# Performance work log

Hardware: AMD Instinct MI355X
Metric: run time of the kernel (lower is better)

Reference implementation:

```python
import jax, jax.numpy as jnp
import numpy as np

NUM_TOKENS = 200


def setup_inputs() -> dict:
    key = jax.random.key(0)
    ks = jax.random.split(key, 4)
    B, N, D, H, O = 16, 4096, 1024, 512, 4096
    x = jax.random.normal(ks[0], (B, N, D), dtype=jnp.float32)
    W1 = jax.random.normal(ks[1], (H, D), dtype=jnp.float32) * (1.0 / np.sqrt(D))
    b1 = jnp.zeros((H,), dtype=jnp.float32)
    W2 = jax.random.normal(ks[2], (1, H), dtype=jnp.float32) * (1.0 / np.sqrt(H))
    b2 = jnp.zeros((1,), dtype=jnp.float32)
    Wp = jax.random.normal(ks[3], (O, D), dtype=jnp.float32) * (1.0 / np.sqrt(D))
    bp = jnp.zeros((O,), dtype=jnp.float32)
    return {"x": x, "W1": W1, "b1": b1, "W2": W2, "b2": b2, "Wp": Wp, "bp": bp}


def reference(x, W1, b1, W2, b2, Wp, bp):
    # score MLP: Linear(D, D//2) -> GELU(exact) -> Linear(D//2, 1)
    h = jax.nn.gelu(jnp.einsum('bnd,hd->bnh', x, W1) + b1, approximate=False)
    scores = jnp.einsum('bnh,oh->bno', h, W2)[..., 0] + b2[0]  # [B, N]
    # topk (sorted descending, matching torch.topk defaults)
    _, topk_idx = jax.lax.top_k(scores, NUM_TOKENS)  # [B, K]
    # gather selected tokens: [B, K, D]
    select_tokens = jnp.take_along_axis(x, topk_idx[:, :, None], axis=1)
    # final projection
    return jnp.einsum('bkd,od->bko', select_tokens, Wp) + bp
```

## Files before the change

kernel.cpp:

```cpp
#include <hip/hip_runtime.h>
#include <cmath>

#define BB 16
#define NN 4096
#define DD 1024
#define HH 512
#define OO 4096
#define KSEL 200
#define NCAND 256
#define NT (BB * NN)
#define NSLOT (BB * NCAND)

typedef __bf16 bf16x8 __attribute__((ext_vector_type(8)));
typedef float floatx4 __attribute__((ext_vector_type(4)));

__device__ __forceinline__ unsigned short f2b(float f) {
    union { float f; unsigned u; } v; v.f = f;
    unsigned r = v.u + 0x7fffu + ((v.u >> 16) & 1u);
    return (unsigned short)(r >> 16);
}
__device__ __forceinline__ unsigned pk2(float lo, float hi) {
    return (unsigned)f2b(lo) | ((unsigned)f2b(hi) << 16);
}

__device__ __forceinline__ float fast_gelu(float u) {
    float z = u * fmaf(0.0713548162726f, u * u, 1.5957691216f);
    float e = __expf(z);
    float r = __builtin_amdgcn_rcpf(e + 1.0f);
    return u - u * r;
}

__device__ __forceinline__ void gl16(const void* g, void* l) {
    __builtin_amdgcn_global_load_lds(
        (const __attribute__((address_space(1))) unsigned int*)g,
        (__attribute__((address_space(3))) unsigned int*)l, 16, 0, 0);
}

__global__ __launch_bounds__(256) void convert_bf16(
    const float* __restrict__ src, unsigned short* __restrict__ dst, int n8)
{
    int i = blockIdx.x * 256 + threadIdx.x;
    if (i >= n8) return;
    float4 a = ((const float4*)src)[2 * i];
    float4 b = ((const float4*)src)[2 * i + 1];
    uint4 o = make_uint4(pk2(a.x, a.y), pk2(a.z, a.w), pk2(b.x, b.y), pk2(b.z, b.w));
    ((uint4*)dst)[i] = o;
}

#define BK 64
#define NSCORE_BLK ((HH / 128) * (NT / 128))

__global__ __launch_bounds__(256) void score_mfma(
    const unsigned short* __restrict__ xb, const unsigned short* __restrict__ W1b,
    const float* __restrict__ b1, const float* __restrict__ W2,
    float* __restrict__ partials)
{
    __shared__ __align__(16) unsigned short As[128 * BK];
    __shared__ __align__(16) unsigned short Bs[128 * BK];
    __shared__ float red[2][128];

    const int tid = threadIdx.x;
    const int bid = blockIdx.x;
    const int swz = (bid & 7) * (NSCORE_BLK / 8) + (bid >> 3);
    const int ht = swz & 3;
    const int h0 = ht * 128;
    const int t0 = (swz >> 2) * 128;

    const int lane = tid & 63;
    const int w = tid >> 6;
    const int wr = w & 1, wc = w >> 1;
    const int l15 = lane & 15, q = lane >> 4;

    const int srow = tid >> 3;
    const int cb = (tid & 7) ^ (srow & 7);
    const unsigned short* pA[4];
    const unsigned short* pB[4];
#pragma unroll
    for (int i = 0; i < 4; ++i) {
        pA[i] = xb  + (size_t)(t0 + i * 32 + srow) * DD + cb * 8;
        pB[i] = W1b + (size_t)(h0 + i * 32 + srow) * DD + cb * 8;
    }

    floatx4 acc[4][4];
#pragma unroll
    for (int mi = 0; mi < 4; ++mi)
#pragma unroll
        for (int ni = 0; ni < 4; ++ni) acc[mi][ni] = (floatx4){0.f, 0.f, 0.f, 0.f};

    for (int kc = 0; kc < DD; kc += BK) {
        __syncthreads();
#pragma unroll
        for (int i = 0; i < 4; ++i) {
            gl16(pA[i] + kc, &As[(i * 256 + w * 64) * 8]);
            gl16(pB[i] + kc, &Bs[(i * 256 + w * 64) * 8]);
        }
        __syncthreads();
#pragma unroll
        for (int kk = 0; kk < BK; kk += 32) {
            const int kb = kk >> 3;
            bf16x8 af[4], bf[4];
#pragma unroll
            for (int mi = 0; mi < 4; ++mi) {
                const int r = wr * 64 + mi * 16 + l15;
                af[mi] = *(const bf16x8*)&As[r * BK + (((kb + q) ^ (r & 7)) << 3)];
            }
#pragma unroll
            for (int ni = 0; ni < 4; ++ni) {
                const int r = wc * 64 + ni * 16 + l15;
                bf[ni] = *(const bf16x8*)&Bs[r * BK + (((kb + q) ^ (r & 7)) << 3)];
            }
#pragma unroll
            for (int mi = 0; mi < 4; ++mi)
#pragma unroll
                for (int ni = 0; ni < 4; ++ni)
                    acc[mi][ni] = __builtin_amdgcn_mfma_f32_16x16x32_bf16(af[mi], bf[ni], acc[mi][ni], 0, 0, 0);
        }
    }

    float s[4][4];
#pragma unroll
    for (int mi = 0; mi < 4; ++mi)
#pragma unroll
        for (int r = 0; r < 4; ++r) s[mi][r] = 0.f;
#pragma unroll
    for (int ni = 0; ni < 4; ++ni) {
        const int n = h0 + wc * 64 + ni * 16 + l15;
        const float bias = b1[n];
        const float w2v = W2[n];
#pragma unroll
        for (int mi = 0; mi < 4; ++mi)
#pragma unroll
            for (int r = 0; r < 4; ++r) {
                float u = acc[mi][ni][r] + bias;
                s[mi][r] = fmaf(fast_gelu(u), w2v, s[mi][r]);
            }
    }
#pragma unroll
    for (int mi = 0; mi < 4; ++mi)
#pragma unroll
        for (int r = 0; r < 4; ++r) {
#pragma unroll
            for (int off = 1; off < 16; off <<= 1)
                s[mi][r] += __shfl_xor(s[mi][r], off, 64);
        }
    __syncthreads();
    if (l15 == 0) {
#pragma unroll
        for (int mi = 0; mi < 4; ++mi)
#pragma unroll
            for (int r = 0; r < 4; ++r)
                red[wc][wr * 64 + mi * 16 + q * 4 + r] = s[mi][r];
    }
    __syncthreads();
    if (tid < 128)
        partials[(size_t)ht * NT + t0 + tid] = red[0][tid] + red[1][tid];
}

__global__ __launch_bounds__(256) void cand_select(
    const float* __restrict__ partials, int* __restrict__ cand)
{
    __shared__ unsigned uk[NN];
    __shared__ int hist[256];
    __shared__ int eq[64];
    __shared__ int sh_pref, sh_rk, sh_cntgt, sh_eqcnt;
    const int b = blockIdx.x, tid = threadIdx.x;

    for (int i = tid; i < NN; i += 256) {
        const int t = b * NN + i;
        float v = partials[t] + partials[NT + t] + partials[2 * NT + t] + partials[3 * NT + t];
        union { float f; unsigned u; } c; c.f = v;
        uk[i] = (c.u & 0x80000000u) ? ~c.u : (c.u | 0x80000000u);
    }
    if (tid == 0) { sh_pref = 0; sh_rk = NCAND; }
    __syncthreads();

    for (int sh = 24; sh >= 0; sh -= 8) {
        hist[tid] = 0;
        __syncthreads();
        const unsigned pref = (unsigned)sh_pref;
        for (int i = tid; i < NN; i += 256) {
            unsigned k = uk[i];
            bool match = (sh == 24) || (((k ^ pref) >> (sh + 8)) == 0);
            if (match) atomicAdd(&hist[(k >> sh) & 255], 1);
        }
        __syncthreads();
        if (tid == 0) {
            int rk = sh_rk, cum = 0;
            for (int bin = 255; bin >= 0; --bin) {
                int c = hist[bin];
                if (cum + c >= rk) { sh_pref = (int)(pref | ((unsigned)bin << sh)); sh_rk = rk - cum; break; }
                cum += c;
            }
        }
        __syncthreads();
    }
    const unsigned T = (unsigned)sh_pref;
    if (tid == 0) { sh_cntgt = 0; sh_eqcnt = 0; }
    cand[b * NCAND + tid] = 0;
    __syncthreads();
    for (int i = tid; i < NN; i += 256) {
        unsigned k = uk[i];
        if (k > T) {
            int p = atomicAdd(&sh_cntgt, 1);
            if (p < NCAND) cand[b * NCAND + p] = i;
        } else if (k == T) {
            int p = atomicAdd(&sh_eqcnt, 1);
            if (p < 64) eq[p] = i;
        }
    }
    __syncthreads();
    if (tid == 0) {
        int cg = sh_cntgt; if (cg > NCAND) cg = NCAND;
        int ec = sh_eqcnt; if (ec > 64) ec = 64;
        int need = NCAND - cg; if (need > ec) need = ec; if (need < 0) need = 0;
        for (int a = 1; a < ec; ++a) {
            int v = eq[a]; int j = a - 1;
            while (j >= 0 && eq[j] > v) { eq[j + 1] = eq[j]; --j; }
            eq[j + 1] = v;
        }
        for (int j = 0; j < need; ++j) cand[b * NCAND + cg + j] = eq[j];
    }
}

#define RT 64
#define RLDP 68

__global__ __launch_bounds__(256) void rescore_kernel(
    const float* __restrict__ x, const int* __restrict__ cand,
    const float* __restrict__ W1, const float* __restrict__ b1,
    const float* __restrict__ W2, float* __restrict__ pc)
{
    __shared__ float As[16][RLDP];
    __shared__ float Bs[16][RLDP];
    __shared__ int rowbase[RT];

    const int tid = threadIdx.x;
    const int s0 = blockIdx.x * RT;
    const int h0 = blockIdx.y * RT;
    const int tx = tid & 15;
    const int ty = tid >> 4;
    const int lr = tid >> 2;
    const int lq = tid & 3;

    if (tid < RT) {
        const int slot = s0 + tid;
        rowbase[tid] = (slot >> 8) * NN + (cand[slot] & (NN - 1));
    }
    __syncthreads();

    const float* Arow = x + (size_t)rowbase[lr] * DD;
    const float* Brow = W1 + (size_t)(h0 + lr) * DD;

    float acc[4][4];
#pragma unroll
    for (int i = 0; i < 4; ++i)
#pragma unroll
        for (int j = 0; j < 4; ++j) acc[i][j] = 0.0f;

    for (int kc = 0; kc < DD; kc += 16) {
        float4 a = *(const float4*)(Arow + kc + lq * 4);
        float4 wv = *(const float4*)(Brow + kc + lq * 4);
        __syncthreads();
        As[lq * 4 + 0][lr] = a.x; As[lq * 4 + 1][lr] = a.y;
        As[lq * 4 + 2][lr] = a.z; As[lq * 4 + 3][lr] = a.w;
        Bs[lq * 4 + 0][lr] = wv.x; Bs[lq * 4 + 1][lr] = wv.y;
        Bs[lq * 4 + 2][lr] = wv.z; Bs[lq * 4 + 3][lr] = wv.w;
        __syncthreads();
#pragma unroll
        for (int kk = 0; kk < 16; ++kk) {
            float ra[4], rb[4];
            *(float4*)&ra[0] = *(const float4*)&As[kk][ty * 4];
            *(float4*)&rb[0] = *(const float4*)&Bs[kk][tx * 4];
#pragma unroll
            for (int i = 0; i < 4; ++i)
#pragma unroll
                for (int j = 0; j < 4; ++j)
                    acc[i][j] = fmaf(ra[i], rb[j], acc[i][j]);
        }
    }

    float s[4];
#pragma unroll
    for (int i = 0; i < 4; ++i) s[i] = 0.0f;
#pragma unroll
    for (int j = 0; j < 4; ++j) {
        const int h = h0 + tx * 4 + j;
        const float bias = b1[h];
        const float w2v = W2[h];
#pragma unroll
        for (int i = 0; i < 4; ++i) {
            float u = acc[i][j] + bias;
            float g = 0.5f * u * (1.0f + erff(u * 0.70710678118654752440f));
            s[i] = fmaf(g, w2v, s[i]);
        }
    }
#pragma unroll
    for (int i = 0; i < 4; ++i) {
#pragma unroll
        for (int off = 8; off > 0; off >>= 1)
            s[i] += __shfl_down(s[i], off, 16);
    }
    if (tx == 0) {
#pragma unroll
        for (int i = 0; i < 4; ++i)
            pc[(size_t)blockIdx.y * NSLOT + s0 + ty * 4 + i] = s[i];
    }
}

__global__ __launch_bounds__(256) void final_topk(
    const float* __restrict__ pc, const int* __restrict__ cand,
    int* __restrict__ topk)
{
    __shared__ unsigned long long keys[NCAND];
    const int b = blockIdx.x, tid = threadIdx.x;
    const int slot = b * NCAND + tid;
    float es = 0.f;
#pragma unroll
    for (int g = 0; g < 8; ++g) es += pc[(size_t)g * NSLOT + slot];
    const int tok = cand[slot];
    union { float f; unsigned u; } c; c.f = es;
    unsigned mono = (c.u & 0x80000000u) ? ~c.u : (c.u | 0x80000000u);
    keys[tid] = ((unsigned long long)mono << 12) | (unsigned)(4095 - tok);
    __syncthreads();

    for (int k = 2; k <= NCAND; k <<= 1) {
        for (int j = k >> 1; j > 0; j >>= 1) {
            const int p = tid ^ j;
            const unsigned long long a = keys[tid];
            const unsigned long long o = keys[p];
            const unsigned long long hi = a > o ? a : o;
            const unsigned long long lo = a > o ? o : a;
            const unsigned long long nv = ((tid < p) == ((tid & k) == 0)) ? hi : lo;
            __syncthreads();
            keys[tid] = nv;
            __syncthreads();
        }
    }
    if (tid < KSEL) topk[b * KSEL + tid] = 4095 - (int)(keys[tid] & 4095u);
}

#define NPROJ_BLK (((BB * KSEL) / 128) * (OO / 128))

__global__ __launch_bounds__(256) void proj_mfma(
    const unsigned short* __restrict__ xb, const int* __restrict__ topk,
    const unsigned short* __restrict__ Wpb, const float* __restrict__ bp,
    float* __restrict__ out)
{
    __shared__ __align__(16) unsigned short As[128 * BK];
    __shared__ __align__(16) unsigned short Bs[128 * BK];
    __shared__ int rowbase[128];

    const int tid = threadIdx.x;
    const int bid = blockIdx.x;
    const int swz = (bid & 7) * (NPROJ_BLK / 8) + (bid >> 3);
    const int r0 = (swz >> 5) * 128;
    const int o0 = (swz & 31) * 128;
    const int lane = tid & 63;
    const int w = tid >> 6;
    const int wr = w & 1, wc = w >> 1;
    const int l15 = lane & 15, q = lane >> 4;

    if (tid < 128) {
        const int r = r0 + tid;
        rowbase[tid] = (r / KSEL) * NN + (topk[r] & (NN - 1));
    }
    __syncthreads();

    const int srow = tid >> 3;
    const int cb = (tid & 7) ^ (srow & 7);
    const unsigned short* pA[4];
    const unsigned short* pB[4];
#pragma unroll
    for (int i = 0; i < 4; ++i) {
        pA[i] = xb  + (size_t)rowbase[i * 32 + srow] * DD + cb * 8;
        pB[i] = Wpb + (size_t)(o0 + i * 32 + srow) * DD + cb * 8;
    }

    floatx4 acc[4][4];
#pragma unroll
    for (int mi = 0; mi < 4; ++mi)
#pragma unroll
        for (int ni = 0; ni < 4; ++ni) acc[mi][ni] = (floatx4){0.f, 0.f, 0.f, 0.f};

    for (int kc = 0; kc < DD; kc += BK) {
        __syncthreads();
#pragma unroll
        for (int i = 0; i < 4; ++i) {
            gl16(pA[i] + kc, &As[(i * 256 + w * 64) * 8]);
            gl16(pB[i] + kc, &Bs[(i * 256 + w * 64) * 8]);
        }
        __syncthreads();
#pragma unroll
        for (int kk = 0; kk < BK; kk += 32) {
            const int kb = kk >> 3;
            bf16x8 af[4], bf[4];
#pragma unroll
            for (int mi = 0; mi < 4; ++mi) {
                const int r = wr * 64 + mi * 16 + l15;
                af[mi] = *(const bf16x8*)&As[r * BK + (((kb + q) ^ (r & 7)) << 3)];
            }
#pragma unroll
            for (int ni = 0; ni < 4; ++ni) {
                const int r = wc * 64 + ni * 16 + l15;
                bf[ni] = *(const bf16x8*)&Bs[r * BK + (((kb + q) ^ (r & 7)) << 3)];
            }
#pragma unroll
            for (int mi = 0; mi < 4; ++mi)
#pragma unroll
                for (int ni = 0; ni < 4; ++ni)
                    acc[mi][ni] = __builtin_amdgcn_mfma_f32_16x16x32_bf16(af[mi], bf[ni], acc[mi][ni], 0, 0, 0);
        }
    }

    float bpv[4];
#pragma unroll
    for (int ni = 0; ni < 4; ++ni) bpv[ni] = bp[o0 + wc * 64 + ni * 16 + l15];
#pragma unroll
    for (int mi = 0; mi < 4; ++mi)
#pragma unroll
        for (int r = 0; r < 4; ++r) {
            const size_t row = (size_t)(r0 + wr * 64 + mi * 16 + q * 4 + r) * OO;
#pragma unroll
            for (int ni = 0; ni < 4; ++ni)
                out[row + o0 + wc * 64 + ni * 16 + l15] = acc[mi][ni][r] + bpv[ni];
        }
}

extern "C" void kernel_launch(void* const* d_in, const int* in_sizes, int n_in,
                              void* d_out, int out_size, void* d_ws, size_t ws_size,
                              hipStream_t stream) {
    const float* x  = (const float*)d_in[0];
    const float* W1 = (const float*)d_in[1];
    const float* b1 = (const float*)d_in[2];
    const float* W2 = (const float*)d_in[3];
    const float* Wp = (const float*)d_in[5];
    const float* bp = (const float*)d_in[6];
    float* out = (float*)d_out;

    char* ws = (char*)d_ws;
    unsigned short* xb  = (unsigned short*)(ws);
    unsigned short* W1b = (unsigned short*)(ws + 134217728);
    unsigned short* Wpb = (unsigned short*)(ws + 135266304);
    float* partials     = (float*)(ws + 143654912);
    float* pc           = (float*)(ws + 144703488);
    int*   cand         = (int*)  (ws + 144834560);
    int*   topk         = (int*)  (ws + 144850944);

    convert_bf16<<<dim3((NT * DD / 8) / 256), 256, 0, stream>>>(x, xb, NT * DD / 8);
    convert_bf16<<<dim3((HH * DD / 8) / 256), 256, 0, stream>>>(W1, W1b, HH * DD / 8);
    convert_bf16<<<dim3((OO * DD / 8) / 256), 256, 0, stream>>>(Wp, Wpb, OO * DD / 8);

    score_mfma<<<dim3(NSCORE_BLK), 256, 0, stream>>>(xb, W1b, b1, W2, partials);

    cand_select<<<dim3(BB), 256, 0, stream>>>(partials, cand);

    rescore_kernel<<<dim3(NSLOT / RT, HH / RT), 256, 0, stream>>>(x, cand, W1, b1, W2, pc);

    final_topk<<<dim3(BB), 256, 0, stream>>>(pc, cand, topk);

    proj_mfma<<<dim3(NPROJ_BLK), 256, 0, stream>>>(xb, topk, Wpb, bp, out);
}
```

Baseline: 677.3 us.

## Fuse fp32-to-bf16 conversion of x into double-buffered GEMM loads

Drops the standalone pass that converts all of x to bf16. The score and projection GEMMs now read fp32 x directly, pack it to bf16 in registers and store it into shared memory. Both GEMM main loops also become double-buffered, prefetching the next K tile while the current one feeds the MFMAs. This removes a full read and write of the large activation tensor. In exchange the GEMMs read twice as many bytes of x per tile, use more shared memory and more registers, and convert the same x tile redundantly across h-tiles.

```diff
diff --git a/kernel.cpp b/kernel.cpp
--- a/kernel.cpp
+++ b/kernel.cpp
@@ -51,12 +51,12 @@
 #define NSCORE_BLK ((HH / 128) * (NT / 128))
 
 __global__ __launch_bounds__(256) void score_mfma(
-    const unsigned short* __restrict__ xb, const unsigned short* __restrict__ W1b,
+    const float* __restrict__ x, const unsigned short* __restrict__ W1b,
     const float* __restrict__ b1, const float* __restrict__ W2,
     float* __restrict__ partials)
 {
-    __shared__ __align__(16) unsigned short As[128 * BK];
-    __shared__ __align__(16) unsigned short Bs[128 * BK];
+    __shared__ __align__(16) unsigned short As[2][128 * BK];
+    __shared__ __align__(16) unsigned short Bs[2][128 * BK];
     __shared__ float red[2][128];
 
     const int tid = threadIdx.x;
@@ -73,11 +73,11 @@
 
     const int srow = tid >> 3;
     const int cb = (tid & 7) ^ (srow & 7);
-    const unsigned short* pA[4];
+    const float* pA[4];
     const unsigned short* pB[4];
 #pragma unroll
     for (int i = 0; i < 4; ++i) {
-        pA[i] = xb  + (size_t)(t0 + i * 32 + srow) * DD + cb * 8;
+        pA[i] = x   + (size_t)(t0 + i * 32 + srow) * DD + cb * 8;
         pB[i] = W1b + (size_t)(h0 + i * 32 + srow) * DD + cb * 8;
     }
 
@@ -87,14 +87,39 @@
 #pragma unroll
         for (int ni = 0; ni < 4; ++ni) acc[mi][ni] = (floatx4){0.f, 0.f, 0.f, 0.f};
 
+    {
+        float4 a0[4], a1[4];
+#pragma unroll
+        for (int i = 0; i < 4; ++i) {
+            a0[i] = *(const float4*)(pA[i] + 0);
+            a1[i] = *(const float4*)(pA[i] + 4);
+        }
+#pragma unroll
+        for (int i = 0; i < 4; ++i) gl16(pB[i], &Bs[0][(i * 256 + w * 64) * 8]);
+#pragma unroll
+        for (int i = 0; i < 4; ++i) {
+            uint4 o = make_uint4(pk2(a0[i].x, a0[i].y), pk2(a0[i].z, a0[i].w),
+                                 pk2(a1[i].x, a1[i].y), pk2(a1[i].z, a1[i].w));
+            *(uint4*)&As[0][(i * 256 + tid) * 8] = o;
+        }
+        __syncthreads();
+    }
+
+    int cur = 0;
     for (int kc = 0; kc < DD; kc += BK) {
-        __syncthreads();
-#pragma unroll
-        for (int i = 0; i < 4; ++i) {
-            gl16(pA[i] + kc, &As[(i * 256 + w * 64) * 8]);
-            gl16(pB[i] + kc, &Bs[(i * 256 + w * 64) * 8]);
-        }
-        __syncthreads();
+        const int nxt = cur ^ 1;
+        const bool pf = (kc + BK) < DD;
+        float4 a0[4], a1[4];
+        if (pf) {
+#pragma unroll
+            for (int i = 0; i < 4; ++i) {
+                a0[i] = *(const float4*)(pA[i] + kc + BK);
+                a1[i] = *(const float4*)(pA[i] + kc + BK + 4);
+            }
+#pragma unroll
+            for (int i = 0; i < 4; ++i)
+                gl16(pB[i] + kc + BK, &Bs[nxt][(i * 256 + w * 64) * 8]);
+        }
 #pragma unroll
         for (int kk = 0; kk < BK; kk += 32) {
             const int kb = kk >> 3;
@@ -102,12 +127,12 @@
 #pragma unroll
             for (int mi = 0; mi < 4; ++mi) {
                 const int r = wr * 64 + mi * 16 + l15;
-                af[mi] = *(const bf16x8*)&As[r * BK + (((kb + q) ^ (r & 7)) << 3)];
+                af[mi] = *(const bf16x8*)&As[cur][r * BK + (((kb + q) ^ (r & 7)) << 3)];
             }
 #pragma unroll
             for (int ni = 0; ni < 4; ++ni) {
                 const int r = wc * 64 + ni * 16 + l15;
-                bf[ni] = *(const bf16x8*)&Bs[r * BK + (((kb + q) ^ (r & 7)) << 3)];
+                bf[ni] = *(const bf16x8*)&Bs[cur][r * BK + (((kb + q) ^ (r & 7)) << 3)];
             }
 #pragma unroll
             for (int mi = 0; mi < 4; ++mi)
@@ -115,6 +140,16 @@
                 for (int ni = 0; ni < 4; ++ni)
                     acc[mi][ni] = __builtin_amdgcn_mfma_f32_16x16x32_bf16(af[mi], bf[ni], acc[mi][ni], 0, 0, 0);
         }
+        if (pf) {
+#pragma unroll
+            for (int i = 0; i < 4; ++i) {
+                uint4 o = make_uint4(pk2(a0[i].x, a0[i].y), pk2(a0[i].z, a0[i].w),
+                                     pk2(a1[i].x, a1[i].y), pk2(a1[i].z, a1[i].w));
+                *(uint4*)&As[nxt][(i * 256 + tid) * 8] = o;
+            }
+        }
+        __syncthreads();
+        cur = nxt;
     }
 
     float s[4][4];
@@ -342,12 +377,12 @@
 #define NPROJ_BLK (((BB * KSEL) / 128) * (OO / 128))
 
 __global__ __launch_bounds__(256) void proj_mfma(
-    const unsigned short* __restrict__ xb, const int* __restrict__ topk,
+    const float* __restrict__ x, const int* __restrict__ topk,
     const unsigned short* __restrict__ Wpb, const float* __restrict__ bp,
     float* __restrict__ out)
 {
-    __shared__ __align__(16) unsigned short As[128 * BK];
-    __shared__ __align__(16) unsigned short Bs[128 * BK];
+    __shared__ __align__(16) unsigned short As[2][128 * BK];
+    __shared__ __align__(16) unsigned short Bs[2][128 * BK];
     __shared__ int rowbase[128];
 
     const int tid = threadIdx.x;
@@ -368,11 +403,11 @@
 
     const int srow = tid >> 3;
     const int cb = (tid & 7) ^ (srow & 7);
-    const unsigned short* pA[4];
+    const float* pA[4];
     const unsigned short* pB[4];
 #pragma unroll
     for (int i = 0; i < 4; ++i) {
-        pA[i] = xb  + (size_t)rowbase[i * 32 + srow] * DD + cb * 8;
+        pA[i] = x   + (size_t)rowbase[i * 32 + srow] * DD + cb * 8;
         pB[i] = Wpb + (size_t)(o0 + i * 32 + srow) * DD + cb * 8;
     }
 
@@ -382,14 +417,39 @@
 #pragma unroll
         for (int ni = 0; ni < 4; ++ni) acc[mi][ni] = (floatx4){0.f, 0.f, 0.f, 0.f};
 
+    {
+        float4 a0[4], a1[4];
+#pragma unroll
+        for (int i = 0; i < 4; ++i) {
+            a0[i] = *(const float4*)(pA[i] + 0);
+            a1[i] = *(const float4*)(pA[i] + 4);
+        }
+#pragma unroll
+        for (int i = 0; i < 4; ++i) gl16(pB[i], &Bs[0][(i * 256 + w * 64) * 8]);
+#pragma unroll
+        for (int i = 0; i < 4; ++i) {
+            uint4 o = make_uint4(pk2(a0[i].x, a0[i].y), pk2(a0[i].z, a0[i].w),
+                                 pk2(a1[i].x, a1[i].y), pk2(a1[i].z, a1[i].w));
+            *(uint4*)&As[0][(i * 256 + tid) * 8] = o;
+        }
+        __syncthreads();
+    }
+
+    int cur = 0;
     for (int kc = 0; kc < DD; kc += BK) {
-        __syncthreads();
-#pragma unroll
-        for (int i = 0; i < 4; ++i) {
-            gl16(pA[i] + kc, &As[(i * 256 + w * 64) * 8]);
-            gl16(pB[i] + kc, &Bs[(i * 256 + w * 64) * 8]);
-        }
-        __syncthreads();
+        const int nxt = cur ^ 1;
+        const bool pf = (kc + BK) < DD;
+        float4 a0[4], a1[4];
+        if (pf) {
+#pragma unroll
+            for (int i = 0; i < 4; ++i) {
+                a0[i] = *(const float4*)(pA[i] + kc + BK);
+                a1[i] = *(const float4*)(pA[i] + kc + BK + 4);
+            }
+#pragma unroll
+            for (int i = 0; i < 4; ++i)
+                gl16(pB[i] + kc + BK, &Bs[nxt][(i * 256 + w * 64) * 8]);
+        }
 #pragma unroll
         for (int kk = 0; kk < BK; kk += 32) {
             const int kb = kk >> 3;
@@ -397,12 +457,12 @@
 #pragma unroll
             for (int mi = 0; mi < 4; ++mi) {
                 const int r = wr * 64 + mi * 16 + l15;
-                af[mi] = *(const bf16x8*)&As[r * BK + (((kb + q) ^ (r & 7)) << 3)];
+                af[mi] = *(const bf16x8*)&As[cur][r * BK + (((kb + q) ^ (r & 7)) << 3)];
             }
 #pragma unroll
             for (int ni = 0; ni < 4; ++ni) {
                 const int r = wc * 64 + ni * 16 + l15;
-                bf[ni] = *(const bf16x8*)&Bs[r * BK + (((kb + q) ^ (r & 7)) << 3)];
+                bf[ni] = *(const bf16x8*)&Bs[cur][r * BK + (((kb + q) ^ (r & 7)) << 3)];
             }
 #pragma unroll
             for (int mi = 0; mi < 4; ++mi)
@@ -410,6 +470,16 @@
                 for (int ni = 0; ni < 4; ++ni)
                     acc[mi][ni] = __builtin_amdgcn_mfma_f32_16x16x32_bf16(af[mi], bf[ni], acc[mi][ni], 0, 0, 0);
         }
+        if (pf) {
+#pragma unroll
+            for (int i = 0; i < 4; ++i) {
+                uint4 o = make_uint4(pk2(a0[i].x, a0[i].y), pk2(a0[i].z, a0[i].w),
+                                     pk2(a1[i].x, a1[i].y), pk2(a1[i].z, a1[i].w));
+                *(uint4*)&As[nxt][(i * 256 + tid) * 8] = o;
+            }
+        }
+        __syncthreads();
+        cur = nxt;
     }
 
     float bpv[4];
@@ -438,19 +508,17 @@
     float* out = (float*)d_out;
 
     char* ws = (char*)d_ws;
-    unsigned short* xb  = (unsigned short*)(ws);
-    unsigned short* W1b = (unsigned short*)(ws + 134217728);
-    unsigned short* Wpb = (unsigned short*)(ws + 135266304);
-    float* partials     = (float*)(ws + 143654912);
-    float* pc           = (float*)(ws + 144703488);
-    int*   cand         = (int*)  (ws + 144834560);
-    int*   topk         = (int*)  (ws + 144850944);
-
-    convert_bf16<<<dim3((NT * DD / 8) / 256), 256, 0, stream>>>(x, xb, NT * DD / 8);
+    unsigned short* W1b = (unsigned short*)(ws);
+    unsigned short* Wpb = (unsigned short*)(ws + 1048576);
+    float* partials     = (float*)(ws + 9437184);
+    float* pc           = (float*)(ws + 10485760);
+    int*   cand         = (int*)  (ws + 10616832);
+    int*   topk         = (int*)  (ws + 10633216);
+
     convert_bf16<<<dim3((HH * DD / 8) / 256), 256, 0, stream>>>(W1, W1b, HH * DD / 8);
     convert_bf16<<<dim3((OO * DD / 8) / 256), 256, 0, stream>>>(Wp, Wpb, OO * DD / 8);
 
-    score_mfma<<<dim3(NSCORE_BLK), 256, 0, stream>>>(xb, W1b, b1, W2, partials);
+    score_mfma<<<dim3(NSCORE_BLK), 256, 0, stream>>>(x, W1b, b1, W2, partials);
 
     cand_select<<<dim3(BB), 256, 0, stream>>>(partials, cand);
 
@@ -458,5 +526,5 @@
 
     final_topk<<<dim3(BB), 256, 0, stream>>>(pc, cand, topk);
 
-    proj_mfma<<<dim3(NPROJ_BLK), 256, 0, stream>>>(xb, topk, Wpb, bp, out);
-}
+    proj_mfma<<<dim3(NPROJ_BLK), 256, 0, stream>>>(x, topk, Wpb, bp, out);
+}
```

After: 704.5 us. 1.04x slower.

## Double-buffer LDS tiles with K=32 in score and projection GEMMs

Applied to the files above, without the earlier changes.

Both MFMA GEMM kernels switch from a single 64-wide K tile loaded behind two barriers to two 32-wide LDS buffers. The next tile is prefetched with global_load_lds while the current one is consumed, leaving one barrier per iteration, and the LDS swizzle is redone for the narrower tile. This aims to hide global load latency behind MFMA work, but it doubles the iteration count and halves the compute done per barrier. Correctness relies on the async LDS load completing before the end-of-iteration barrier.

```diff
diff --git a/kernel.cpp b/kernel.cpp
--- a/kernel.cpp
+++ b/kernel.cpp
@@ -47,7 +47,7 @@
     ((uint4*)dst)[i] = o;
 }
 
-#define BK 64
+#define TK 32
 #define NSCORE_BLK ((HH / 128) * (NT / 128))
 
 __global__ __launch_bounds__(256) void score_mfma(
@@ -55,8 +55,8 @@
     const float* __restrict__ b1, const float* __restrict__ W2,
     float* __restrict__ partials)
 {
-    __shared__ __align__(16) unsigned short As[128 * BK];
-    __shared__ __align__(16) unsigned short Bs[128 * BK];
+    __shared__ __align__(16) unsigned short As[2][128 * TK];
+    __shared__ __align__(16) unsigned short Bs[2][128 * TK];
     __shared__ float red[2][128];
 
     const int tid = threadIdx.x;
@@ -71,14 +71,14 @@
     const int wr = w & 1, wc = w >> 1;
     const int l15 = lane & 15, q = lane >> 4;
 
-    const int srow = tid >> 3;
-    const int cb = (tid & 7) ^ (srow & 7);
-    const unsigned short* pA[4];
-    const unsigned short* pB[4];
-#pragma unroll
-    for (int i = 0; i < 4; ++i) {
-        pA[i] = xb  + (size_t)(t0 + i * 32 + srow) * DD + cb * 8;
-        pB[i] = W1b + (size_t)(h0 + i * 32 + srow) * DD + cb * 8;
+    const int srow = tid >> 2;
+    const int cb = (tid & 3) ^ ((tid >> 3) & 3);
+    const unsigned short* pA[2];
+    const unsigned short* pB[2];
+#pragma unroll
+    for (int i = 0; i < 2; ++i) {
+        pA[i] = xb  + (size_t)(t0 + i * 64 + srow) * DD + cb * 8;
+        pB[i] = W1b + (size_t)(h0 + i * 64 + srow) * DD + cb * 8;
     }
 
     floatx4 acc[4][4];
@@ -87,34 +87,41 @@
 #pragma unroll
         for (int ni = 0; ni < 4; ++ni) acc[mi][ni] = (floatx4){0.f, 0.f, 0.f, 0.f};
 
-    for (int kc = 0; kc < DD; kc += BK) {
-        __syncthreads();
-#pragma unroll
-        for (int i = 0; i < 4; ++i) {
-            gl16(pA[i] + kc, &As[(i * 256 + w * 64) * 8]);
-            gl16(pB[i] + kc, &Bs[(i * 256 + w * 64) * 8]);
-        }
-        __syncthreads();
-#pragma unroll
-        for (int kk = 0; kk < BK; kk += 32) {
-            const int kb = kk >> 3;
-            bf16x8 af[4], bf[4];
-#pragma unroll
-            for (int mi = 0; mi < 4; ++mi) {
-                const int r = wr * 64 + mi * 16 + l15;
-                af[mi] = *(const bf16x8*)&As[r * BK + (((kb + q) ^ (r & 7)) << 3)];
+#pragma unroll
+    for (int i = 0; i < 2; ++i) {
+        gl16(pA[i], &As[0][(i * 256 + w * 64) * 8]);
+        gl16(pB[i], &Bs[0][(i * 256 + w * 64) * 8]);
+    }
+    __syncthreads();
+
+    int cur = 0;
+    for (int kc = 0; kc < DD; kc += TK) {
+        const int nxt = cur ^ 1;
+        if (kc + TK < DD) {
+#pragma unroll
+            for (int i = 0; i < 2; ++i) {
+                gl16(pA[i] + kc + TK, &As[nxt][(i * 256 + w * 64) * 8]);
+                gl16(pB[i] + kc + TK, &Bs[nxt][(i * 256 + w * 64) * 8]);
             }
-#pragma unroll
-            for (int ni = 0; ni < 4; ++ni) {
-                const int r = wc * 64 + ni * 16 + l15;
-                bf[ni] = *(const bf16x8*)&Bs[r * BK + (((kb + q) ^ (r & 7)) << 3)];
-            }
-#pragma unroll
-            for (int mi = 0; mi < 4; ++mi)
-#pragma unroll
-                for (int ni = 0; ni < 4; ++ni)
-                    acc[mi][ni] = __builtin_amdgcn_mfma_f32_16x16x32_bf16(af[mi], bf[ni], acc[mi][ni], 0, 0, 0);
-        }
+        }
+        bf16x8 af[4], bf[4];
+#pragma unroll
+        for (int mi = 0; mi < 4; ++mi) {
+            const int r = wr * 64 + mi * 16 + l15;
+            af[mi] = *(const bf16x8*)&As[cur][r * TK + ((q ^ ((r >> 1) & 3)) << 3)];
+        }
+#pragma unroll
+        for (int ni = 0; ni < 4; ++ni) {
+            const int r = wc * 64 + ni * 16 + l15;
+            bf[ni] = *(const bf16x8*)&Bs[cur][r * TK + ((q ^ ((r >> 1) & 3)) << 3)];
+        }
+#pragma unroll
+        for (int mi = 0; mi < 4; ++mi)
+#pragma unroll
+            for (int ni = 0; ni < 4; ++ni)
+                acc[mi][ni] = __builtin_amdgcn_mfma_f32_16x16x32_bf16(af[mi], bf[ni], acc[mi][ni], 0, 0, 0);
+        __syncthreads();
+        cur = nxt;
     }
 
     float s[4][4];
@@ -346,8 +353,8 @@
     const unsigned short* __restrict__ Wpb, const float* __restrict__ bp,
     float* __restrict__ out)
 {
-    __shared__ __align__(16) unsigned short As[128 * BK];
-    __shared__ __align__(16) unsigned short Bs[128 * BK];
+    __shared__ __align__(16) unsigned short As[2][128 * TK];
+    __shared__ __align__(16) unsigned short Bs[2][128 * TK];
     __shared__ int rowbase[128];
 
     const int tid = threadIdx.x;
@@ -366,14 +373,14 @@
     }
     __syncthreads();
 
-    const int srow = tid >> 3;
-    const int cb = (tid & 7) ^ (srow & 7);
-    const unsigned short* pA[4];
-    const unsigned short* pB[4];
-#pragma unroll
-    for (int i = 0; i < 4; ++i) {
-        pA[i] = xb  + (size_t)rowbase[i * 32 + srow] * DD + cb * 8;
-        pB[i] = Wpb + (size_t)(o0 + i * 32 + srow) * DD + cb * 8;
+    const int srow = tid >> 2;
+    const int cb = (tid & 3) ^ ((tid >> 3) & 3);
+    const unsigned short* pA[2];
+    const unsigned short* pB[2];
+#pragma unroll
+    for (int i = 0; i < 2; ++i) {
+        pA[i] = xb  + (size_t)rowbase[i * 64 + srow] * DD + cb * 8;
+        pB[i] = Wpb + (size_t)(o0 + i * 64 + srow) * DD + cb * 8;
     }
 
     floatx4 acc[4][4];
@@ -382,34 +389,41 @@
 #pragma unroll
         for (int ni = 0; ni < 4; ++ni) acc[mi][ni] = (floatx4){0.f, 0.f, 0.f, 0.f};
 
-    for (int kc = 0; kc < DD; kc += BK) {
-        __syncthreads();
-#pragma unroll
-        for (int i = 0; i < 4; ++i) {
-            gl16(pA[i] + kc, &As[(i * 256 + w * 64) * 8]);
-            gl16(pB[i] + kc, &Bs[(i * 256 + w * 64) * 8]);
-        }
-        __syncthreads();
-#pragma unroll
-        for (int kk = 0; kk < BK; kk += 32) {
-            const int kb = kk >> 3;
-            bf16x8 af[4], bf[4];
-#pragma unroll
-            for (int mi = 0; mi < 4; ++mi) {
-                const int r = wr * 64 + mi * 16 + l15;
-                af[mi] = *(const bf16x8*)&As[r * BK + (((kb + q) ^ (r & 7)) << 3)];
+#pragma unroll
+    for (int i = 0; i < 2; ++i) {
+        gl16(pA[i], &As[0][(i * 256 + w * 64) * 8]);
+        gl16(pB[i], &Bs[0][(i * 256 + w * 64) * 8]);
+    }
+    __syncthreads();
+
+    int cur = 0;
+    for (int kc = 0; kc < DD; kc += TK) {
+        const int nxt = cur ^ 1;
+        if (kc + TK < DD) {
+#pragma unroll
+            for (int i = 0; i < 2; ++i) {
+                gl16(pA[i] + kc + TK, &As[nxt][(i * 256 + w * 64) * 8]);
+                gl16(pB[i] + kc + TK, &Bs[nxt][(i * 256 + w * 64) * 8]);
             }
-#pragma unroll
-            for (int ni = 0; ni < 4; ++ni) {
-                const int r = wc * 64 + ni * 16 + l15;
-                bf[ni] = *(const bf16x8*)&Bs[r * BK + (((kb + q) ^ (r & 7)) << 3)];
-            }
-#pragma unroll
-            for (int mi = 0; mi < 4; ++mi)
-#pragma unroll
-                for (int ni = 0; ni < 4; ++ni)
-                    acc[mi][ni] = __builtin_amdgcn_mfma_f32_16x16x32_bf16(af[mi], bf[ni], acc[mi][ni], 0, 0, 0);
-        }
+        }
+        bf16x8 af[4], bf[4];
+#pragma unroll
+        for (int mi = 0; mi < 4; ++mi) {
+            const int r = wr * 64 + mi * 16 + l15;
+            af[mi] = *(const bf16x8*)&As[cur][r * TK + ((q ^ ((r >> 1) & 3)) << 3)];
+        }
+#pragma unroll
+        for (int ni = 0; ni < 4; ++ni) {
+            const int r = wc * 64 + ni * 16 + l15;
+            bf[ni] = *(const bf16x8*)&Bs[cur][r * TK + ((q ^ ((r >> 1) & 3)) << 3)];
+        }
+#pragma unroll
+        for (int mi = 0; mi < 4; ++mi)
+#pragma unroll
+            for (int ni = 0; ni < 4; ++ni)
+                acc[mi][ni] = __builtin_amdgcn_mfma_f32_16x16x32_bf16(af[mi], bf[ni], acc[mi][ni], 0, 0, 0);
+        __syncthreads();
+        cur = nxt;
     }
 
     float bpv[4];
```

New measurement: 679.4 us. No clear change (+0.3%).
